# Kernel optimization log

Measured on AMD Instinct MI355X. Metric: run time of the kernel, lower is better.

The kernel has to match this reference:

```python
import jax, jax.numpy as jnp
import numpy as np

VOCAB, D, H, HK, DH, M, DFF, NCLS = 32000, 512, 8, 2, 64, 64, 2048, 2
G = H // HK  # GQA group size = 4
EPS = 1e-6


def rmsnorm(x, g):
    return x * jax.lax.rsqrt(jnp.mean(x * x, axis=-1, keepdims=True) + EPS) * g


def setup_inputs() -> dict:
    key = jax.random.key(0)
    ks = jax.random.split(key, 14)
    s = 0.02
    return {
        "input_ids": jax.random.randint(ks[0], (8, 8192), 0, VOCAB),
        "emb": jax.random.normal(ks[1], (VOCAB, D), jnp.float32) * s,
        "Wq": jax.random.normal(ks[2], (D, H * DH), jnp.float32) * s,
        "Wk": jax.random.normal(ks[3], (D, HK * DH), jnp.float32) * s,
        "Wv": jax.random.normal(ks[4], (D, HK * DH), jnp.float32) * s,
        "Wphi": jax.random.normal(ks[5], (DH, M), jnp.float32),  # Laplacian kernel feature projection
        "Wo": jax.random.normal(ks[6], (H * DH, D), jnp.float32) * s,
        "g1": jnp.ones((D,), jnp.float32),
        "g2": jnp.ones((D,), jnp.float32),
        "Wg": jax.random.normal(ks[7], (D, DFF), jnp.float32) * s,
        "Wu": jax.random.normal(ks[8], (D, DFF), jnp.float32) * s,  # frozen up_proj (freeze only affects training, not math)
        "Wd": jax.random.normal(ks[9], (DFF, D), jnp.float32) * s,
        "Wc": jax.random.normal(ks[10], (D, NCLS), jnp.float32) * s,
        "bc": jnp.zeros((NCLS,), jnp.float32),
    }


def reference(input_ids, emb, Wq, Wk, Wv, Wphi, Wo, g1, g2, Wg, Wu, Wd, Wc, bc):
    B, S = input_ids.shape
    x = emb[input_ids]  # [B,S,D] embedding gather
    # --- kernelized (Laplacian) bidirectional GQA linear attention, pre-norm ---
    h = rmsnorm(x, g1)
    q = (h @ Wq).reshape(B, S, H, DH)
    k = (h @ Wk).reshape(B, S, HK, DH)
    v = (h @ Wv).reshape(B, S, HK, DH)
    # Laplacian positive feature map: phi(u) = exp(-|u @ Wphi|)  -> [.., M]
    pq = jnp.exp(-jnp.abs(jnp.einsum("bshd,dm->bshm", q, Wphi)))
    pk = jnp.exp(-jnp.abs(jnp.einsum("bskd,dm->bskm", k, Wphi)))
    # global (bidirectional) state per kv head: [B,HK,M,DH] and normalizer [B,HK,M]
    kv = jnp.einsum("bskm,bskd->bkmd", pk, v)
    z = pk.sum(axis=1)
    pqg = pq.reshape(B, S, HK, G, M)  # group query heads onto kv heads
    num = jnp.einsum("bskgm,bkmd->bskgd", pqg, kv)
    den = jnp.einsum("bskgm,bkm->bskg", pqg, z)
    attn = (num / (den[..., None] + EPS)).reshape(B, S, H * DH)
    x = x + attn @ Wo
    # --- SwiGLU FFN, pre-norm ---
    h2 = rmsnorm(x, g2)
    x = x + (jax.nn.silu(h2 @ Wg) * (h2 @ Wu)) @ Wd
    # --- mean pool + linear head ---
    logits = x.mean(axis=1) @ Wc + bc  # [B, NCLS]
    return logits
```

## Files before the change

### kernel.cpp

```cpp
#include <hip/hip_runtime.h>
#include <hip/hip_bf16.h>
#include <math.h>

typedef __attribute__((ext_vector_type(8))) short bf16x8;
typedef __attribute__((ext_vector_type(4))) float f32x4;

#define DEV static __device__ __forceinline__
#define AS1 __attribute__((address_space(1)))
#define AS3 __attribute__((address_space(3)))

DEV float bf2f(__hip_bfloat16 v) { return __bfloat162float(v); }
DEV __hip_bfloat16 f2bf(float f) { return __float2bfloat16(f); }
DEV float us2f(unsigned short u) { return __uint_as_float(((unsigned int)u) << 16); }
DEV unsigned short f2us(float f) {
    __hip_bfloat16 b = __float2bfloat16(f);
    return *(unsigned short*)&b;
}

DEV void gload_lds16(const void* g, void* l) {
    __builtin_amdgcn_global_load_lds((const AS1 unsigned int*)g,
                                     (AS3 unsigned int*)l, 16, 0, 0);
}

DEV void load8(const void* p, size_t off, int f32m, float* o) {
    if (f32m) {
        const float4* r = (const float4*)((const float*)p + off);
        float4 A = r[0], B = r[1];
        o[0] = A.x; o[1] = A.y; o[2] = A.z; o[3] = A.w;
        o[4] = B.x; o[5] = B.y; o[6] = B.z; o[7] = B.w;
    } else {
        const ushort4* r = (const ushort4*)((const __hip_bfloat16*)p + off);
        ushort4 A = r[0], B = r[1];
        o[0] = us2f(A.x); o[1] = us2f(A.y); o[2] = us2f(A.z); o[3] = us2f(A.w);
        o[4] = us2f(B.x); o[5] = us2f(B.y); o[6] = us2f(B.z); o[7] = us2f(B.w);
    }
}

DEV float loadElem(const void* p, size_t idx, int f32m) {
    return f32m ? ((const float*)p)[idx] : bf2f(((const __hip_bfloat16*)p)[idx]);
}

constexpr int NTOK = 65536;

constexpr size_t OFF_WQPT = 0;
constexpr size_t OFF_WKPT = OFF_WQPT + 524288ull;
constexpr size_t OFF_WVT  = OFF_WKPT + 131072ull;
constexpr size_t OFF_WOT  = OFF_WVT  + 131072ull;
constexpr size_t OFF_WGT  = OFF_WOT  + 524288ull;
constexpr size_t OFF_WUT  = OFF_WGT  + 2097152ull;
constexpr size_t OFF_KV   = OFF_WUT  + 2097152ull;
constexpr size_t OFF_Z    = OFF_KV   + 262144ull;
constexpr size_t OFF_POOL = OFF_Z    + 4096ull;
constexpr size_t OFF_TSUM = OFF_POOL + 16384ull;
constexpr size_t OFF_FLAG = OFF_TSUM + 65536ull;
constexpr size_t PERSIST  = OFF_FLAG + 256ull;
constexpr size_t CHUNKBASE = PERSIST;
constexpr int    ZERO_FLOATS = (262144 + 4096 + 16384 + 65536) / 4;
constexpr size_t PERTOK = 4608ull;

__global__ __launch_bounds__(128) void detect_kernel(
    const unsigned int* __restrict__ w, int* __restrict__ flag)
{
    __shared__ int cnt;
    if (threadIdx.x == 0) cnt = 0;
    __syncthreads();
    unsigned int v = w[threadIdx.x];
    float a = fabsf(us2f((unsigned short)(v & 0xFFFFu)));
    if (a >= 0.0625f && a <= 8.0f) atomicAdd(&cnt, 1);
    __syncthreads();
    if (threadIdx.x == 0) *flag = (cnt < 64) ? 1 : 0;
}

__global__ __launch_bounds__(256) void zero_kernel(float* __restrict__ p, int n)
{
    int i = blockIdx.x * 256 + threadIdx.x;
    if (i < n) p[i] = 0.0f;
}

__global__ __launch_bounds__(256) void fuse_phi_kernel(
    const void* __restrict__ W, const void* __restrict__ Wphi,
    __hip_bfloat16* __restrict__ outT, int wld, const int* __restrict__ flag)
{
    const int f = *flag;
    int o = blockIdx.x * 256 + threadIdx.x;
    int hm = o >> 9, d = o & 511;
    int h = hm >> 6, m = hm & 63;
    float acc = 0.f;
    if (f) {
        const float* Wf = (const float*)W;
        const float* Pf = (const float*)Wphi;
        #pragma unroll 8
        for (int dh = 0; dh < 64; ++dh)
            acc += Wf[(size_t)d * wld + h * 64 + dh] * Pf[dh * 64 + m];
    } else {
        const __hip_bfloat16* Wb = (const __hip_bfloat16*)W;
        const __hip_bfloat16* Pb = (const __hip_bfloat16*)Wphi;
        #pragma unroll 8
        for (int dh = 0; dh < 64; ++dh)
            acc += bf2f(Wb[(size_t)d * wld + h * 64 + dh]) * bf2f(Pb[dh * 64 + m]);
    }
    outT[o] = f2bf(acc);
}

__global__ __launch_bounds__(256) void transpose_kernel(
    const void* __restrict__ src, __hip_bfloat16* __restrict__ dst, int R, int Ccols,
    const int* __restrict__ flag)
{
    __shared__ float tile[32][33];
    const int f = *flag;
    const int tx = threadIdx.x & 31, ty = threadIdx.x >> 5;
    const int c0 = blockIdx.x * 32, r0 = blockIdx.y * 32;
    #pragma unroll
    for (int k = 0; k < 4; ++k) {
        const int rl = ty + k * 8;
        tile[rl][tx] = loadElem(src, (size_t)(r0 + rl) * Ccols + c0 + tx, f);
    }
    __syncthreads();
    #pragma unroll
    for (int k = 0; k < 4; ++k) {
        const int cl = ty + k * 8;
        dst[(size_t)(c0 + cl) * R + r0 + tx] = f2bf(tile[tx][cl]);
    }
}

__global__ __launch_bounds__(256) void embed_rms_kernel(
    const int* __restrict__ ids, const void* __restrict__ emb,
    const void* __restrict__ g1, __hip_bfloat16* __restrict__ h,
    const int* __restrict__ flag)
{
    const int f = *flag;
    const int n = blockIdx.x * 4 + (threadIdx.x >> 6);
    const int lane = threadIdx.x & 63;
    const int id = ids[n];
    float x[8];
    load8(emb, (size_t)id * 512 + lane * 8, f, x);
    float ss = 0.f;
    #pragma unroll
    for (int i = 0; i < 8; ++i) ss += x[i] * x[i];
    #pragma unroll
    for (int off = 32; off; off >>= 1) ss += __shfl_xor(ss, off, 64);
    const float scale = rsqrtf(ss * (1.0f / 512.0f) + 1e-6f);
    float gv[8];
    load8(g1, (size_t)lane * 8, f, gv);
    ushort4 h0, h1;
    h0.x = f2us(x[0] * scale * gv[0]); h0.y = f2us(x[1] * scale * gv[1]);
    h0.z = f2us(x[2] * scale * gv[2]); h0.w = f2us(x[3] * scale * gv[3]);
    h1.x = f2us(x[4] * scale * gv[4]); h1.y = f2us(x[5] * scale * gv[5]);
    h1.z = f2us(x[6] * scale * gv[6]); h1.w = f2us(x[7] * scale * gv[7]);
    ushort4* ho = (ushort4*)(h + (size_t)n * 512 + lane * 8);
    ho[0] = h0; ho[1] = h1;
}

__global__ __launch_bounds__(256) void rms2_kernel(
    const float* __restrict__ xf, const void* __restrict__ g2,
    __hip_bfloat16* __restrict__ h, const int* __restrict__ flag)
{
    const int f = *flag;
    const int n = blockIdx.x * 4 + (threadIdx.x >> 6);
    const int lane = threadIdx.x & 63;
    const float4* xr = (const float4*)(xf + (size_t)n * 512);
    float4 a = xr[lane * 2], b = xr[lane * 2 + 1];
    float x[8] = { a.x, a.y, a.z, a.w, b.x, b.y, b.z, b.w };
    float ss = 0.f;
    #pragma unroll
    for (int i = 0; i < 8; ++i) ss += x[i] * x[i];
    #pragma unroll
    for (int off = 32; off; off >>= 1) ss += __shfl_xor(ss, off, 64);
    const float scale = rsqrtf(ss * (1.0f / 512.0f) + 1e-6f);
    float gv[8];
    load8(g2, (size_t)lane * 8, f, gv);
    ushort4 h0, h1;
    h0.x = f2us(x[0] * scale * gv[0]); h0.y = f2us(x[1] * scale * gv[1]);
    h0.z = f2us(x[2] * scale * gv[2]); h0.w = f2us(x[3] * scale * gv[3]);
    h1.x = f2us(x[4] * scale * gv[4]); h1.y = f2us(x[5] * scale * gv[5]);
    h1.z = f2us(x[6] * scale * gv[6]); h1.w = f2us(x[7] * scale * gv[7]);
    ushort4* ho = (ushort4*)(h + (size_t)n * 512 + lane * 8);
    ho[0] = h0; ho[1] = h1;
}

template<int MODE>
__global__ __launch_bounds__(256) void gemm128_kernel(
    const __hip_bfloat16* __restrict__ A, const __hip_bfloat16* __restrict__ Bt,
    float* __restrict__ xf, __hip_bfloat16* __restrict__ Cout2,
    float* __restrict__ pooled, const int* __restrict__ ids,
    const void* __restrict__ emb, const int* __restrict__ flag, int gbase, int K)
{
    __shared__ __align__(16) char As[8192];
    __shared__ __align__(16) char Bs[8192];
    __shared__ int idsL[128];

    const int tid = threadIdx.x;
    const int bm = blockIdx.x, bn = blockIdx.y;
    const int wave = tid >> 6, lane = tid & 63;
    const int quad = lane >> 4, lr = lane & 15;
    const int wm = (wave >> 1) << 6, wn = (wave & 1) << 6;

    if (MODE == 7 && tid < 128) idsL[tid] = ids[bm * 128 + tid];

    const int srow = (wave << 5) + (lane >> 2);
    const int scol = lane & 3;
    const int sfr  = (srow + (srow >> 2)) & 3;
    const int sofs = ((scol ^ sfr) << 3);

    const __hip_bfloat16* ga0 = A  + (size_t)(bm * 128 + srow) * K + sofs;
    const __hip_bfloat16* gb0 = Bt + (size_t)(bn * 128 + srow) * K + sofs;
    const __hip_bfloat16* ga1 = ga0 + (size_t)16 * K;
    const __hip_bfloat16* gb1 = gb0 + (size_t)16 * K;
    char* lA0 = As + (wave << 11);
    char* lA1 = lA0 + 1024;
    char* lB0 = Bs + (wave << 11);
    char* lB1 = lB0 + 1024;

    const int fl  = (lr + (lr >> 2)) & 3;
    const int ac  = (quad ^ fl) << 4;
    const char* arp = As + ((wm + lr) << 6) + ac;
    const char* brp = Bs + ((wn + lr) << 6) + ac;

    f32x4 acc[4][4];
    #pragma unroll
    for (int i = 0; i < 4; ++i)
        #pragma unroll
        for (int j = 0; j < 4; ++j)
            #pragma unroll
            for (int r = 0; r < 4; ++r) acc[i][j][r] = 0.0f;

    for (int k0 = 0; k0 < K; k0 += 32) {
        __syncthreads();
        gload_lds16(ga0 + k0, lA0);
        gload_lds16(ga1 + k0, lA1);
        gload_lds16(gb0 + k0, lB0);
        gload_lds16(gb1 + k0, lB1);
        __syncthreads();

        bf16x8 af[4], bfr[4];
        #pragma unroll
        for (int i = 0; i < 4; ++i)
            af[i] = *(const bf16x8*)(arp + i * 1024);
        #pragma unroll
        for (int j = 0; j < 4; ++j)
            bfr[j] = *(const bf16x8*)(brp + j * 1024);
        #pragma unroll
        for (int i = 0; i < 4; ++i)
            #pragma unroll
            for (int j = 0; j < 4; ++j)
                acc[i][j] = __builtin_amdgcn_mfma_f32_16x16x32_bf16(af[i], bfr[j], acc[i][j], 0, 0, 0);
    }

    const int col0 = bn * 128 + wn + lr;

    if (MODE == 7) {
        const int f = *flag;
        const int b = (gbase + bm * 128) >> 13;
        #pragma unroll
        for (int j = 0; j < 4; ++j) {
            const int col = col0 + j * 16;
            float s = 0.f;
            #pragma unroll
            for (int i = 0; i < 4; ++i)
                #pragma unroll
                for (int r = 0; r < 4; ++r) {
                    const int rl = wm + i * 16 + quad * 4 + r;
                    const float e = loadElem(emb, (size_t)idsL[rl] * 512 + col, f);
                    const float w = e + acc[i][j][r];
                    xf[(size_t)(bm * 128 + rl) * 512 + col] = w;
                    s += w;
                }
            s += __shfl_xor(s, 16, 64);
            s += __shfl_xor(s, 32, 64);
            if (quad == 0) atomicAdd(&pooled[b * 512 + col], s);
        }
        return;
    }

    const int row0 = bm * 128 + wm + quad * 4;
    #pragma unroll
    for (int i = 0; i < 4; ++i)
        #pragma unroll
        for (int j = 0; j < 4; ++j) {
            const int col = col0 + j * 16;
            #pragma unroll
            for (int r = 0; r < 4; ++r) {
                const int row = row0 + i * 16 + r;
                const float v = acc[i][j][r];
                Cout2[(size_t)row * 256 + col] = f2bf(bn == 0 ? expf(-fabsf(v)) : v);
            }
        }
}

__global__ __launch_bounds__(256, 2) void pq_mix_kernel(
    const __hip_bfloat16* __restrict__ h, const __hip_bfloat16* __restrict__ WQPt,
    const float* __restrict__ kvf, const float* __restrict__ zf,
    __hip_bfloat16* __restrict__ attn, int gbase, int K)
{
    __shared__ __align__(16) char As[8192];
    __shared__ __align__(16) char Bs[8192];
    __shared__ __align__(16) char Pl[128 * 272];
    __shared__ __align__(16) __hip_bfloat16 kvT[80][72];

    const int tid = threadIdx.x;
    const int bm = blockIdx.x, bn = blockIdx.y;
    const int kh = bn >> 1;
    const int wave = tid >> 6, lane = tid & 63;
    const int quad = lane >> 4, lr = lane & 15;
    const int wm = (wave >> 1) << 6, wn = (wave & 1) << 6;
    const int b = (gbase + bm * 128) >> 13;

    {
        const float* kvsrc = kvf + ((size_t)b * 2 + kh) * 4096;
        for (int i = tid; i < 4096; i += 256) {
            const int m = i >> 6, dh = i & 63;
            kvT[dh][m] = f2bf(kvsrc[i]);
        }
        if (tid < 64) kvT[64][tid] = f2bf(zf[((size_t)b * 2 + kh) * 64 + tid]);
        for (int i = tid; i < 15 * 64; i += 256)
            kvT[65 + (i >> 6)][i & 63] = f2bf(0.0f);
    }

    const int srow = (wave << 5) + (lane >> 2);
    const int scol = lane & 3;
    const int sfr  = (srow + (srow >> 2)) & 3;
    const int sofs = ((scol ^ sfr) << 3);

    const __hip_bfloat16* ga0 = h    + (size_t)(bm * 128 + srow) * K + sofs;
    const __hip_bfloat16* gb0 = WQPt + (size_t)(bn * 128 + srow) * K + sofs;
    const __hip_bfloat16* ga1 = ga0 + (size_t)16 * K;
    const __hip_bfloat16* gb1 = gb0 + (size_t)16 * K;
    char* lA0 = As + (wave << 11);
    char* lA1 = lA0 + 1024;
    char* lB0 = Bs + (wave << 11);
    char* lB1 = lB0 + 1024;

    const int fl  = (lr + (lr >> 2)) & 3;
    const int ac  = (quad ^ fl) << 4;
    const char* arp = As + ((wm + lr) << 6) + ac;
    const char* brp = Bs + ((wn + lr) << 6) + ac;

    f32x4 acc[4][4];
    #pragma unroll
    for (int i = 0; i < 4; ++i)
        #pragma unroll
        for (int j = 0; j < 4; ++j)
            #pragma unroll
            for (int r = 0; r < 4; ++r) acc[i][j][r] = 0.0f;

    for (int k0 = 0; k0 < K; k0 += 32) {
        __syncthreads();
        gload_lds16(ga0 + k0, lA0);
        gload_lds16(ga1 + k0, lA1);
        gload_lds16(gb0 + k0, lB0);
        gload_lds16(gb1 + k0, lB1);
        __syncthreads();

        bf16x8 af[4], bfr[4];
        #pragma unroll
        for (int i = 0; i < 4; ++i)
            af[i] = *(const bf16x8*)(arp + i * 1024);
        #pragma unroll
        for (int j = 0; j < 4; ++j)
            bfr[j] = *(const bf16x8*)(brp + j * 1024);
        #pragma unroll
        for (int i = 0; i < 4; ++i)
            #pragma unroll
            for (int j = 0; j < 4; ++j)
                acc[i][j] = __builtin_amdgcn_mfma_f32_16x16x32_bf16(af[i], bfr[j], acc[i][j], 0, 0, 0);
    }

    #pragma unroll
    for (int i = 0; i < 4; ++i)
        #pragma unroll
        for (int j = 0; j < 4; ++j)
            #pragma unroll
            for (int r = 0; r < 4; ++r) {
                const int rl = wm + i * 16 + quad * 4 + r;
                const int cl = wn + j * 16 + lr;
                *(__hip_bfloat16*)(Pl + rl * 272 + cl * 2) = f2bf(expf(-fabsf(acc[i][j][r])));
            }
    __syncthreads();

    const int hl = wave & 1;
    f32x4 acc2[4][5];
    #pragma unroll
    for (int i = 0; i < 4; ++i)
        #pragma unroll
        for (int j = 0; j < 5; ++j)
            #pragma unroll
            for (int r = 0; r < 4; ++r) acc2[i][j][r] = 0.0f;

    #pragma unroll
    for (int kk = 0; kk < 2; ++kk) {
        const int kofs = kk * 32 + quad * 8;
        bf16x8 af[4], bfr[5];
        #pragma unroll
        for (int i = 0; i < 4; ++i)
            af[i] = *(const bf16x8*)(Pl + (wm + i * 16 + lr) * 272 + (wn + kofs) * 2);
        #pragma unroll
        for (int j = 0; j < 5; ++j)
            bfr[j] = *(const bf16x8*)&kvT[j * 16 + lr][kofs];
        #pragma unroll
        for (int i = 0; i < 4; ++i)
            #pragma unroll
            for (int j = 0; j < 5; ++j)
                acc2[i][j] = __builtin_amdgcn_mfma_f32_16x16x32_bf16(af[i], bfr[j], acc2[i][j], 0, 0, 0);
    }

    const int colb = (bn * 2 + hl) * 64;
    #pragma unroll
    for (int i = 0; i < 4; ++i) {
        const int rowb = bm * 128 + wm + i * 16 + quad * 4;
        #pragma unroll
        for (int r = 0; r < 4; ++r) {
            const float den = __shfl(acc2[i][4][r], lane & 48, 64);
            const float inv = 1.0f / (den + 1e-6f);
            const size_t base = (size_t)(rowb + r) * 512 + colb;
            #pragma unroll
            for (int j = 0; j < 4; ++j)
                attn[base + j * 16 + lr] = f2bf(acc2[i][j][r] * inv);
        }
    }
}

__global__ __launch_bounds__(256, 2) void gemm_ffn_kernel(
    const __hip_bfloat16* __restrict__ A, const __hip_bfloat16* __restrict__ Bg,
    const __hip_bfloat16* __restrict__ Bu, float* __restrict__ tsum,
    int gbase, int K)
{
    __shared__ __align__(16) char As[16384];
    __shared__ __align__(16) char Gs[16384];
    __shared__ __align__(16) char Us[16384];

    const int tid = threadIdx.x;
    const int bm = blockIdx.x, bn = blockIdx.y;
    const int wave = tid >> 6, lane = tid & 63;
    const int quad = lane >> 4, lr = lane & 15;
    const int wm = (wave >> 1) << 6, wn = (wave & 1) << 6;

    const int srow = (wave << 5) + (lane >> 2);
    const int scol = lane & 3;
    const int sfr  = (srow + (srow >> 2)) & 3;
    const int sofs = ((scol ^ sfr) << 3);

    const __hip_bfloat16* ga0 = A  + (size_t)(bm * 128 + srow) * K + sofs;
    const __hip_bfloat16* gg0 = Bg + (size_t)(bn * 128 + srow) * K + sofs;
    const __hip_bfloat16* gu0 = Bu + (size_t)(bn * 128 + srow) * K + sofs;
    const __hip_bfloat16* ga1 = ga0 + (size_t)16 * K;
    const __hip_bfloat16* gg1 = gg0 + (size_t)16 * K;
    const __hip_bfloat16* gu1 = gu0 + (size_t)16 * K;
    char* lA0 = As + (wave << 11);
    char* lG0 = Gs + (wave << 11);
    char* lU0 = Us + (wave << 11);

    const int fl  = (lr + (lr >> 2)) & 3;
    const int ac  = (quad ^ fl) << 4;
    const char* arp = As + ((wm + lr) << 6) + ac;
    const char* grp = Gs + ((wn + lr) << 6) + ac;
    const char* urp = Us + ((wn + lr) << 6) + ac;

    f32x4 accG[4][4], accU[4][4];
    #pragma unroll
    for (int i = 0; i < 4; ++i)
        #pragma unroll
        for (int j = 0; j < 4; ++j)
            #pragma unroll
            for (int r = 0; r < 4; ++r) { accG[i][j][r] = 0.0f; accU[i][j][r] = 0.0f; }

    for (int k0 = 0; k0 < K; k0 += 64) {
        __syncthreads();
        gload_lds16(ga0 + k0,      lA0);
        gload_lds16(ga1 + k0,      lA0 + 1024);
        gload_lds16(ga0 + k0 + 32, lA0 + 8192);
        gload_lds16(ga1 + k0 + 32, lA0 + 8192 + 1024);
        gload_lds16(gg0 + k0,      lG0);
        gload_lds16(gg1 + k0,      lG0 + 1024);
        gload_lds16(gg0 + k0 + 32, lG0 + 8192);
        gload_lds16(gg1 + k0 + 32, lG0 + 8192 + 1024);
        gload_lds16(gu0 + k0,      lU0);
        gload_lds16(gu1 + k0,      lU0 + 1024);
        gload_lds16(gu0 + k0 + 32, lU0 + 8192);
        gload_lds16(gu1 + k0 + 32, lU0 + 8192 + 1024);
        __syncthreads();

        #pragma unroll
        for (int kk = 0; kk < 2; ++kk) {
            const int so = kk * 8192;
            bf16x8 af[4], bgf[4], buf_[4];
            #pragma unroll
            for (int i = 0; i < 4; ++i)
                af[i] = *(const bf16x8*)(arp + so + i * 1024);
            #pragma unroll
            for (int j = 0; j < 4; ++j) {
                bgf[j]  = *(const bf16x8*)(grp + so + j * 1024);
                buf_[j] = *(const bf16x8*)(urp + so + j * 1024);
            }
            #pragma unroll
            for (int i = 0; i < 4; ++i)
                #pragma unroll
                for (int j = 0; j < 4; ++j) {
                    accG[i][j] = __builtin_amdgcn_mfma_f32_16x16x32_bf16(af[i], bgf[j],  accG[i][j], 0, 0, 0);
                    accU[i][j] = __builtin_amdgcn_mfma_f32_16x16x32_bf16(af[i], buf_[j], accU[i][j], 0, 0, 0);
                }
        }
    }

    const int b = (gbase + bm * 128) >> 13;
    #pragma unroll
    for (int j = 0; j < 4; ++j) {
        float s = 0.f;
        #pragma unroll
        for (int i = 0; i < 4; ++i)
            #pragma unroll
            for (int r = 0; r < 4; ++r) {
                const float g = accG[i][j][r];
                s += (g / (1.0f + expf(-g))) * accU[i][j][r];
            }
        s += __shfl_xor(s, 16, 64);
        s += __shfl_xor(s, 32, 64);
        if (quad == 0)
            atomicAdd(&tsum[b * 2048 + bn * 128 + wn + lr + j * 16], s);
    }
}

__global__ __launch_bounds__(256) void ffn_pool_kernel(
    const float* __restrict__ tsum, const void* __restrict__ Wd,
    float* __restrict__ pooled, const int* __restrict__ flag)
{
    __shared__ float ts[8][64];
    const int f = *flag;
    const int k0 = blockIdx.x * 64;
    const int t = threadIdx.x;
    for (int i = t; i < 512; i += 256)
        ts[i >> 6][i & 63] = tsum[(i >> 6) * 2048 + k0 + (i & 63)];
    __syncthreads();

    float acc0[8] = {}, acc1[8] = {};
    for (int kk = 0; kk < 64; ++kk) {
        const size_t krow = (size_t)(k0 + kk) * 512;
        const float w0 = loadElem(Wd, krow + t, f);
        const float w1 = loadElem(Wd, krow + t + 256, f);
        #pragma unroll
        for (int b = 0; b < 8; ++b) {
            acc0[b] += ts[b][kk] * w0;
            acc1[b] += ts[b][kk] * w1;
        }
    }
    #pragma unroll
    for (int b = 0; b < 8; ++b) {
        atomicAdd(&pooled[b * 512 + t], acc0[b]);
        atomicAdd(&pooled[b * 512 + t + 256], acc1[b]);
    }
}

__global__ __launch_bounds__(256) void kv_z_kernel(
    const __hip_bfloat16* __restrict__ pkv,
    float* __restrict__ kv, float* __restrict__ z, int gbase, int nrows)
{
    __shared__ float pks[8][64], vs[8][64];
    const int slab = blockIdx.x, kh = blockIdx.y;
    const int b = (gbase + slab * nrows) >> 13;
    const int tid = threadIdx.x;
    const int tm = (tid & 15) << 2, tdh = (tid >> 4) << 2;
    const int lss = tid >> 5, lmm = (tid & 31) << 1;

    float acc[4][4] = {};
    float zacc[4] = {};
    for (int sb = 0; sb < nrows; sb += 8) {
        __syncthreads();
        {
            const size_t n = (size_t)slab * nrows + sb + lss;
            const __hip_bfloat16* pr = pkv + n * 256 + kh * 64 + lmm;
            const __hip_bfloat16* vr = pkv + n * 256 + 128 + kh * 64 + lmm;
            pks[lss][lmm]     = bf2f(pr[0]);
            pks[lss][lmm + 1] = bf2f(pr[1]);
            vs[lss][lmm]      = bf2f(vr[0]);
            vs[lss][lmm + 1]  = bf2f(vr[1]);
        }
        __syncthreads();
        #pragma unroll
        for (int ss = 0; ss < 8; ++ss) {
            f32x4 p = *(const f32x4*)&pks[ss][tm];
            f32x4 w = *(const f32x4*)&vs[ss][tdh];
            #pragma unroll
            for (int i = 0; i < 4; ++i)
                #pragma unroll
                for (int j = 0; j < 4; ++j)
                    acc[i][j] += p[i] * w[j];
            if ((tid >> 4) == 0) {
                #pragma unroll
                for (int i = 0; i < 4; ++i) zacc[i] += p[i];
            }
        }
    }
    #pragma unroll
    for (int i = 0; i < 4; ++i)
        #pragma unroll
        for (int j = 0; j < 4; ++j)
            atomicAdd(&kv[(((size_t)b * 2 + kh) * 64 + tm + i) * 64 + tdh + j], acc[i][j]);
    if ((tid >> 4) == 0) {
        #pragma unroll
        for (int i = 0; i < 4; ++i)
            atomicAdd(&z[((size_t)b * 2 + kh) * 64 + tm + i], zacc[i]);
    }
}

__global__ __launch_bounds__(256) void head_kernel(
    const float* __restrict__ pooled, const void* __restrict__ Wc,
    const void* __restrict__ bc, void* __restrict__ out, const int* __restrict__ flag)
{
    const int f = *flag;
    const int t = threadIdx.x;
    const int grp = t >> 4, ln = t & 15;
    const int b = grp >> 1, c = grp & 1;
    float p = 0.f;
    for (int d = ln; d < 512; d += 16)
        p += pooled[b * 512 + d] * loadElem(Wc, (size_t)d * 2 + c, f);
    #pragma unroll
    for (int off = 8; off; off >>= 1) p += __shfl_xor(p, off, 64);
    if (ln == 0) {
        const float val = p * (1.0f / 8192.0f) + loadElem(bc, c, f);
        if (f) ((float*)out)[b * 2 + c] = val;
        else   ((__hip_bfloat16*)out)[b * 2 + c] = f2bf(val);
    }
}

extern "C" void kernel_launch(void* const* d_in, const int* in_sizes, int n_in,
                              void* d_out, int out_size, void* d_ws, size_t ws_size,
                              hipStream_t stream)
{
    const int* ids   = (const int*)d_in[0];
    const void* emb  = d_in[1];
    const void* Wq   = d_in[2];
    const void* Wk   = d_in[3];
    const void* Wv   = d_in[4];
    const void* Wph  = d_in[5];
    const void* Wo   = d_in[6];
    const void* g1   = d_in[7];
    const void* g2   = d_in[8];
    const void* Wg   = d_in[9];
    const void* Wu   = d_in[10];
    const void* Wd   = d_in[11];
    const void* Wc   = d_in[12];
    const void* bc   = d_in[13];

    char* ws = (char*)d_ws;
    __hip_bfloat16* WQPt  = (__hip_bfloat16*)(ws + OFF_WQPT);
    __hip_bfloat16* WKPt  = (__hip_bfloat16*)(ws + OFF_WKPT);
    __hip_bfloat16* WvT   = (__hip_bfloat16*)(ws + OFF_WVT);
    __hip_bfloat16* WoT   = (__hip_bfloat16*)(ws + OFF_WOT);
    __hip_bfloat16* WgT   = (__hip_bfloat16*)(ws + OFF_WGT);
    __hip_bfloat16* WuT   = (__hip_bfloat16*)(ws + OFF_WUT);
    float*          kv    = (float*)(ws + OFF_KV);
    float*          z     = (float*)(ws + OFF_Z);
    float*          pooled= (float*)(ws + OFF_POOL);
    float*          tsum  = (float*)(ws + OFF_TSUM);
    int*            flag  = (int*)(ws + OFF_FLAG);

    int C = 32768;
    while (C > 256 && CHUNKBASE + PERTOK * (size_t)C > ws_size) C >>= 1;
    const int NC = NTOK / C;

    char* cb = ws + CHUNKBASE;
    float*          xf   = (float*)cb;
    __hip_bfloat16* h    = (__hip_bfloat16*)(cb + (size_t)C * 2048);
    __hip_bfloat16* attn = (__hip_bfloat16*)(cb + (size_t)C * 3072);
    __hip_bfloat16* pkv  = (__hip_bfloat16*)(cb + (size_t)C * 4096);

    detect_kernel<<<1, 128, 0, stream>>>((const unsigned int*)Wph, flag);
    zero_kernel<<<(ZERO_FLOATS + 255) / 256, 256, 0, stream>>>(kv, ZERO_FLOATS);

    fuse_phi_kernel<<<1024, 256, 0, stream>>>(Wq, Wph, WQPt, 512, flag);
    fuse_phi_kernel<<<256, 256, 0, stream>>>(Wk, Wph, WKPt, 128, flag);
    transpose_kernel<<<dim3(128 / 32, 512 / 32), 256, 0, stream>>>(Wv, WvT, 512, 128, flag);
    transpose_kernel<<<dim3(512 / 32, 512 / 32), 256, 0, stream>>>(Wo, WoT, 512, 512, flag);
    transpose_kernel<<<dim3(2048 / 32, 512 / 32), 256, 0, stream>>>(Wg, WgT, 512, 2048, flag);
    transpose_kernel<<<dim3(2048 / 32, 512 / 32), 256, 0, stream>>>(Wu, WuT, 512, 2048, flag);

    for (int c = 0; c < NC; ++c) {
        const int g0 = c * C;
        embed_rms_kernel<<<C / 4, 256, 0, stream>>>(ids + g0, emb, g1, h, flag);
        gemm128_kernel<8><<<dim3(C / 128, 2), 256, 0, stream>>>(
            h, WKPt, nullptr, pkv, nullptr, nullptr, nullptr, flag, g0, 512);
        kv_z_kernel<<<dim3(C / 128, 2), 256, 0, stream>>>(pkv, kv, z, g0, 128);
    }

    for (int c = 0; c < NC; ++c) {
        const int g0 = c * C;
        embed_rms_kernel<<<C / 4, 256, 0, stream>>>(ids + g0, emb, g1, h, flag);
        pq_mix_kernel<<<dim3(C / 128, 4), 256, 0, stream>>>(
            h, WQPt, kv, z, attn, g0, 512);
        gemm128_kernel<7><<<dim3(C / 128, 4), 256, 0, stream>>>(
            attn, WoT, xf, nullptr, pooled, ids + g0, emb, flag, g0, 512);
        rms2_kernel<<<C / 4, 256, 0, stream>>>(xf, g2, h, flag);
        dim3 gg(C / 128, 16);
        gemm_ffn_kernel<<<gg, 256, 0, stream>>>(h, WgT, WuT, tsum, g0, 512);
    }

    ffn_pool_kernel<<<32, 256, 0, stream>>>(tsum, Wd, pooled, flag);

    head_kernel<<<1, 256, 0, stream>>>(pooled, Wc, bc, d_out, flag);
}
```

Measured before the change: 968.6 us.

## Rewrite FFN GEMM as 8-wave double-buffered kernel and cache normalized activations

Replaces the 256-thread gate/up FFN GEMM with a 512-thread, 256x128 tile kernel. It double-buffers LDS across K steps, staggers global-to-LDS loads between phases, and raises MFMA priority with s_setprio. Each wave computes both gate and up columns in one accumulator array. It also stores the first-pass RMS-normalized activations for the full token range in a persistent buffer, so the second pass no longer re-runs embed_rms. The cost is 64 MB more workspace, which may shrink the chunk size, and 128 KB of LDS per block, which limits occupancy.

```diff
diff --git a/kernel.cpp b/kernel.cpp
--- a/kernel.cpp
+++ b/kernel.cpp
@@ -54,9 +54,10 @@
 constexpr size_t OFF_TSUM = OFF_POOL + 16384ull;
 constexpr size_t OFF_FLAG = OFF_TSUM + 65536ull;
 constexpr size_t PERSIST  = OFF_FLAG + 256ull;
-constexpr size_t CHUNKBASE = PERSIST;
+constexpr size_t OFF_H    = PERSIST;
+constexpr size_t CHUNKBASE = OFF_H + 67108864ull;
 constexpr int    ZERO_FLOATS = (262144 + 4096 + 16384 + 65536) / 4;
-constexpr size_t PERTOK = 4608ull;
+constexpr size_t PERTOK = 3584ull;
 
 __global__ __launch_bounds__(128) void detect_kernel(
     const unsigned int* __restrict__ w, int* __restrict__ flag)
@@ -419,103 +420,151 @@
     }
 }
 
-__global__ __launch_bounds__(256, 2) void gemm_ffn_kernel(
+__global__ __launch_bounds__(512, 2) void ffn8_kernel(
     const __hip_bfloat16* __restrict__ A, const __hip_bfloat16* __restrict__ Bg,
-    const __hip_bfloat16* __restrict__ Bu, float* __restrict__ tsum,
-    int gbase, int K)
-{
-    __shared__ __align__(16) char As[16384];
-    __shared__ __align__(16) char Gs[16384];
-    __shared__ __align__(16) char Us[16384];
+    const __hip_bfloat16* __restrict__ Bu, float* __restrict__ tsum, int gbase)
+{
+    __shared__ __align__(16) char L[131072];
 
     const int tid = threadIdx.x;
     const int bm = blockIdx.x, bn = blockIdx.y;
     const int wave = tid >> 6, lane = tid & 63;
     const int quad = lane >> 4, lr = lane & 15;
-    const int wm = (wave >> 1) << 6, wn = (wave & 1) << 6;
-
-    const int srow = (wave << 5) + (lane >> 2);
-    const int scol = lane & 3;
-    const int sfr  = (srow + (srow >> 2)) & 3;
-    const int sofs = ((scol ^ sfr) << 3);
-
-    const __hip_bfloat16* ga0 = A  + (size_t)(bm * 128 + srow) * K + sofs;
-    const __hip_bfloat16* gg0 = Bg + (size_t)(bn * 128 + srow) * K + sofs;
-    const __hip_bfloat16* gu0 = Bu + (size_t)(bn * 128 + srow) * K + sofs;
-    const __hip_bfloat16* ga1 = ga0 + (size_t)16 * K;
-    const __hip_bfloat16* gg1 = gg0 + (size_t)16 * K;
-    const __hip_bfloat16* gu1 = gu0 + (size_t)16 * K;
-    char* lA0 = As + (wave << 11);
-    char* lG0 = Gs + (wave << 11);
-    char* lU0 = Us + (wave << 11);
-
-    const int fl  = (lr + (lr >> 2)) & 3;
-    const int ac  = (quad ^ fl) << 4;
-    const char* arp = As + ((wm + lr) << 6) + ac;
-    const char* grp = Gs + ((wn + lr) << 6) + ac;
-    const char* urp = Us + ((wn + lr) << 6) + ac;
-
-    f32x4 accG[4][4], accU[4][4];
-    #pragma unroll
-    for (int i = 0; i < 4; ++i)
+    const int wm = (wave >> 2) << 7;
+    const int wn = (wave & 3) << 5;
+
+    const int trow = tid >> 3;
+    const int cswz = (((tid & 7) ^ (trow & 7)) << 3);
+    const __hip_bfloat16* gA0 = A  + (size_t)(bm * 256 + trow) * 512 + cswz;
+    const __hip_bfloat16* gG0 = Bg + (size_t)(bn * 128 + trow) * 512 + cswz;
+    const __hip_bfloat16* gU0 = Bu + (size_t)(bn * 128 + trow) * 512 + cswz;
+    const int ldsb = wave << 10;
+
+    const int sx = lr & 7;
+    const int s0 = (quad ^ sx) << 4;
+    const int s1 = ((quad + 4) ^ sx) << 4;
+    const int aro = (wm + lr) << 7;
+    const int bgo = 32768 + ((wn + lr) << 7);
+    const int buo = bgo + 16384;
+
+    f32x4 acc[8][4];
+    #pragma unroll
+    for (int m = 0; m < 8; ++m)
         #pragma unroll
         for (int j = 0; j < 4; ++j)
             #pragma unroll
-            for (int r = 0; r < 4; ++r) { accG[i][j][r] = 0.0f; accU[i][j][r] = 0.0f; }
-
-    for (int k0 = 0; k0 < K; k0 += 64) {
-        __syncthreads();
-        gload_lds16(ga0 + k0,      lA0);
-        gload_lds16(ga1 + k0,      lA0 + 1024);
-        gload_lds16(ga0 + k0 + 32, lA0 + 8192);
-        gload_lds16(ga1 + k0 + 32, lA0 + 8192 + 1024);
-        gload_lds16(gg0 + k0,      lG0);
-        gload_lds16(gg1 + k0,      lG0 + 1024);
-        gload_lds16(gg0 + k0 + 32, lG0 + 8192);
-        gload_lds16(gg1 + k0 + 32, lG0 + 8192 + 1024);
-        gload_lds16(gu0 + k0,      lU0);
-        gload_lds16(gu1 + k0,      lU0 + 1024);
-        gload_lds16(gu0 + k0 + 32, lU0 + 8192);
-        gload_lds16(gu1 + k0 + 32, lU0 + 8192 + 1024);
-        __syncthreads();
-
-        #pragma unroll
-        for (int kk = 0; kk < 2; ++kk) {
-            const int so = kk * 8192;
-            bf16x8 af[4], bgf[4], buf_[4];
-            #pragma unroll
-            for (int i = 0; i < 4; ++i)
-                af[i] = *(const bf16x8*)(arp + so + i * 1024);
-            #pragma unroll
-            for (int j = 0; j < 4; ++j) {
-                bgf[j]  = *(const bf16x8*)(grp + so + j * 1024);
-                buf_[j] = *(const bf16x8*)(urp + so + j * 1024);
-            }
-            #pragma unroll
-            for (int i = 0; i < 4; ++i)
-                #pragma unroll
-                for (int j = 0; j < 4; ++j) {
-                    accG[i][j] = __builtin_amdgcn_mfma_f32_16x16x32_bf16(af[i], bgf[j],  accG[i][j], 0, 0, 0);
-                    accU[i][j] = __builtin_amdgcn_mfma_f32_16x16x32_bf16(af[i], buf_[j], accU[i][j], 0, 0, 0);
-                }
-        }
-    }
-
-    const int b = (gbase + bm * 128) >> 13;
-    #pragma unroll
-    for (int j = 0; j < 4; ++j) {
+            for (int r = 0; r < 4; ++r) acc[m][j][r] = 0.0f;
+
+    #pragma unroll
+    for (int l = 0; l < 4; ++l)
+        gload_lds16(gA0 + (size_t)l * 32768, L + l * 8192 + ldsb);
+    gload_lds16(gG0,         L + 32768 + ldsb);
+    gload_lds16(gG0 + 32768, L + 40960 + ldsb);
+    gload_lds16(gU0,         L + 49152 + ldsb);
+    gload_lds16(gU0 + 32768, L + 57344 + ldsb);
+
+    for (int t = 0; t < 8; ++t) {
+        const char* cbuf = L + ((t & 1) << 16);
+        char* nbuf = (char*)L + (((t + 1) & 1) << 16);
+        const int kn = (t + 1) << 6;
+        bf16x8 af[4], bfv[4];
+
+        if (t < 7) {
+            #pragma unroll
+            for (int l = 0; l < 4; ++l)
+                gload_lds16(gA0 + (size_t)l * 32768 + kn, nbuf + l * 8192 + ldsb);
+            asm volatile("s_waitcnt vmcnt(4)" ::: "memory");
+        } else {
+            asm volatile("s_waitcnt vmcnt(0)" ::: "memory");
+        }
+        __builtin_amdgcn_s_barrier();
+        asm volatile("" ::: "memory");
+        #pragma unroll
+        for (int m = 0; m < 4; ++m) af[m] = *(const bf16x8*)(cbuf + aro + m * 2048 + s0);
+        bfv[0] = *(const bf16x8*)(cbuf + bgo + s0);
+        bfv[1] = *(const bf16x8*)(cbuf + bgo + 2048 + s0);
+        bfv[2] = *(const bf16x8*)(cbuf + buo + s0);
+        bfv[3] = *(const bf16x8*)(cbuf + buo + 2048 + s0);
+        asm volatile("s_waitcnt lgkmcnt(0)" ::: "memory");
+        __builtin_amdgcn_s_setprio(1);
+        #pragma unroll
+        for (int m = 0; m < 4; ++m)
+            #pragma unroll
+            for (int j = 0; j < 4; ++j)
+                acc[m][j] = __builtin_amdgcn_mfma_f32_16x16x32_bf16(af[m], bfv[j], acc[m][j], 0, 0, 0);
+        __builtin_amdgcn_s_setprio(0);
+        asm volatile("" ::: "memory");
+        __builtin_amdgcn_s_barrier();
+        asm volatile("" ::: "memory");
+
+        if (t < 7) {
+            gload_lds16(gG0 + kn,         nbuf + 32768 + ldsb);
+            gload_lds16(gG0 + 32768 + kn, nbuf + 40960 + ldsb);
+            gload_lds16(gU0 + kn,         nbuf + 49152 + ldsb);
+            gload_lds16(gU0 + 32768 + kn, nbuf + 57344 + ldsb);
+        }
+        #pragma unroll
+        for (int m = 0; m < 4; ++m) af[m] = *(const bf16x8*)(cbuf + aro + (m + 4) * 2048 + s0);
+        asm volatile("s_waitcnt lgkmcnt(0)" ::: "memory");
+        __builtin_amdgcn_s_setprio(1);
+        #pragma unroll
+        for (int m = 0; m < 4; ++m)
+            #pragma unroll
+            for (int j = 0; j < 4; ++j)
+                acc[m + 4][j] = __builtin_amdgcn_mfma_f32_16x16x32_bf16(af[m], bfv[j], acc[m + 4][j], 0, 0, 0);
+        __builtin_amdgcn_s_setprio(0);
+        asm volatile("" ::: "memory");
+        __builtin_amdgcn_s_barrier();
+        asm volatile("" ::: "memory");
+
+        #pragma unroll
+        for (int m = 0; m < 4; ++m) af[m] = *(const bf16x8*)(cbuf + aro + m * 2048 + s1);
+        bfv[0] = *(const bf16x8*)(cbuf + bgo + s1);
+        bfv[1] = *(const bf16x8*)(cbuf + bgo + 2048 + s1);
+        bfv[2] = *(const bf16x8*)(cbuf + buo + s1);
+        bfv[3] = *(const bf16x8*)(cbuf + buo + 2048 + s1);
+        asm volatile("s_waitcnt lgkmcnt(0)" ::: "memory");
+        __builtin_amdgcn_s_setprio(1);
+        #pragma unroll
+        for (int m = 0; m < 4; ++m)
+            #pragma unroll
+            for (int j = 0; j < 4; ++j)
+                acc[m][j] = __builtin_amdgcn_mfma_f32_16x16x32_bf16(af[m], bfv[j], acc[m][j], 0, 0, 0);
+        __builtin_amdgcn_s_setprio(0);
+        asm volatile("" ::: "memory");
+        __builtin_amdgcn_s_barrier();
+        asm volatile("" ::: "memory");
+
+        #pragma unroll
+        for (int m = 0; m < 4; ++m) af[m] = *(const bf16x8*)(cbuf + aro + (m + 4) * 2048 + s1);
+        asm volatile("s_waitcnt lgkmcnt(0)" ::: "memory");
+        __builtin_amdgcn_s_setprio(1);
+        #pragma unroll
+        for (int m = 0; m < 4; ++m)
+            #pragma unroll
+            for (int j = 0; j < 4; ++j)
+                acc[m + 4][j] = __builtin_amdgcn_mfma_f32_16x16x32_bf16(af[m], bfv[j], acc[m + 4][j], 0, 0, 0);
+        __builtin_amdgcn_s_setprio(0);
+        asm volatile("" ::: "memory");
+        __builtin_amdgcn_s_barrier();
+        asm volatile("" ::: "memory");
+    }
+
+    const int b = (gbase + bm * 256) >> 13;
+    #pragma unroll
+    for (int j = 0; j < 2; ++j) {
         float s = 0.f;
         #pragma unroll
-        for (int i = 0; i < 4; ++i)
+        for (int m = 0; m < 8; ++m)
             #pragma unroll
             for (int r = 0; r < 4; ++r) {
-                const float g = accG[i][j][r];
-                s += (g / (1.0f + expf(-g))) * accU[i][j][r];
+                const float g = acc[m][j][r];
+                s += (g / (1.0f + expf(-g))) * acc[m][j + 2][r];
             }
         s += __shfl_xor(s, 16, 64);
         s += __shfl_xor(s, 32, 64);
         if (quad == 0)
-            atomicAdd(&tsum[b * 2048 + bn * 128 + wn + lr + j * 16], s);
+            atomicAdd(&tsum[b * 2048 + bn * 128 + wn + j * 16 + lr], s);
     }
 }
 
@@ -652,6 +701,7 @@
     float*          pooled= (float*)(ws + OFF_POOL);
     float*          tsum  = (float*)(ws + OFF_TSUM);
     int*            flag  = (int*)(ws + OFF_FLAG);
+    __hip_bfloat16* hall  = (__hip_bfloat16*)(ws + OFF_H);
 
     int C = 32768;
     while (C > 256 && CHUNKBASE + PERTOK * (size_t)C > ws_size) C >>= 1;
@@ -659,9 +709,8 @@
 
     char* cb = ws + CHUNKBASE;
     float*          xf   = (float*)cb;
-    __hip_bfloat16* h    = (__hip_bfloat16*)(cb + (size_t)C * 2048);
-    __hip_bfloat16* attn = (__hip_bfloat16*)(cb + (size_t)C * 3072);
-    __hip_bfloat16* pkv  = (__hip_bfloat16*)(cb + (size_t)C * 4096);
+    __hip_bfloat16* attn = (__hip_bfloat16*)(cb + (size_t)C * 2048);
+    __hip_bfloat16* pkv  = (__hip_bfloat16*)(cb + (size_t)C * 3072);
 
     detect_kernel<<<1, 128, 0, stream>>>((const unsigned int*)Wph, flag);
     zero_kernel<<<(ZERO_FLOATS + 255) / 256, 256, 0, stream>>>(kv, ZERO_FLOATS);
@@ -675,22 +724,22 @@
 
     for (int c = 0; c < NC; ++c) {
         const int g0 = c * C;
-        embed_rms_kernel<<<C / 4, 256, 0, stream>>>(ids + g0, emb, g1, h, flag);
+        __hip_bfloat16* hc = hall + (size_t)g0 * 512;
+        embed_rms_kernel<<<C / 4, 256, 0, stream>>>(ids + g0, emb, g1, hc, flag);
         gemm128_kernel<8><<<dim3(C / 128, 2), 256, 0, stream>>>(
-            h, WKPt, nullptr, pkv, nullptr, nullptr, nullptr, flag, g0, 512);
+            hc, WKPt, nullptr, pkv, nullptr, nullptr, nullptr, flag, g0, 512);
         kv_z_kernel<<<dim3(C / 128, 2), 256, 0, stream>>>(pkv, kv, z, g0, 128);
     }
 
     for (int c = 0; c < NC; ++c) {
         const int g0 = c * C;
-        embed_rms_kernel<<<C / 4, 256, 0, stream>>>(ids + g0, emb, g1, h, flag);
+        __hip_bfloat16* hc = hall + (size_t)g0 * 512;
         pq_mix_kernel<<<dim3(C / 128, 4), 256, 0, stream>>>(
-            h, WQPt, kv, z, attn, g0, 512);
+            hc, WQPt, kv, z, attn, g0, 512);
         gemm128_kernel<7><<<dim3(C / 128, 4), 256, 0, stream>>>(
             attn, WoT, xf, nullptr, pooled, ids + g0, emb, flag, g0, 512);
-        rms2_kernel<<<C / 4, 256, 0, stream>>>(xf, g2, h, flag);
-        dim3 gg(C / 128, 16);
-        gemm_ffn_kernel<<<gg, 256, 0, stream>>>(h, WgT, WuT, tsum, g0, 512);
+        rms2_kernel<<<C / 4, 256, 0, stream>>>(xf, g2, hc, flag);
+        ffn8_kernel<<<dim3(C / 256, 16), 512, 0, stream>>>(hc, WgT, WuT, tsum, g0);
     }
 
     ffn_pool_kernel<<<32, 256, 0, stream>>>(tsum, Wd, pooled, flag);
```

After: 963.2 us. About the same (-0.6%).

## Keep normed activations across passes and restructure FFN GEMM with full-K A tile in LDS

Applied to the files above, without the earlier changes.

The normed hidden states from the first pass are now stored in a persistent 64MB buffer, so the second pass no longer recomputes the embedding gather and RMSNorm. The FFN gate/up GEMM is rewritten so that each 512-thread block loads its full 128x512 A tile into 128KB of LDS once. Each of its 8 waves then streams Wg/Wu columns directly from global memory and covers the whole 2048-wide FFN width, which removes re-reading A from global memory for each of 16 N-tiles. The costs are much higher LDS use (one block per CU), B operands read from global without LDS staging, a larger workspace requirement that may force smaller chunks, and fewer blocks in the grid.

```diff
diff --git a/kernel.cpp b/kernel.cpp
--- a/kernel.cpp
+++ b/kernel.cpp
@@ -54,9 +54,10 @@
 constexpr size_t OFF_TSUM = OFF_POOL + 16384ull;
 constexpr size_t OFF_FLAG = OFF_TSUM + 65536ull;
 constexpr size_t PERSIST  = OFF_FLAG + 256ull;
-constexpr size_t CHUNKBASE = PERSIST;
+constexpr size_t OFF_H    = PERSIST;
+constexpr size_t CHUNKBASE = OFF_H + 67108864ull;
 constexpr int    ZERO_FLOATS = (262144 + 4096 + 16384 + 65536) / 4;
-constexpr size_t PERTOK = 4608ull;
+constexpr size_t PERTOK = 3584ull;
 
 __global__ __launch_bounds__(128) void detect_kernel(
     const unsigned int* __restrict__ w, int* __restrict__ flag)
@@ -419,103 +420,85 @@
     }
 }
 
-__global__ __launch_bounds__(256, 2) void gemm_ffn_kernel(
+__global__ __launch_bounds__(512, 2) void ffn8_kernel(
     const __hip_bfloat16* __restrict__ A, const __hip_bfloat16* __restrict__ Bg,
-    const __hip_bfloat16* __restrict__ Bu, float* __restrict__ tsum,
-    int gbase, int K)
-{
-    __shared__ __align__(16) char As[16384];
-    __shared__ __align__(16) char Gs[16384];
-    __shared__ __align__(16) char Us[16384];
+    const __hip_bfloat16* __restrict__ Bu, float* __restrict__ tsum, int gbase)
+{
+    __shared__ __align__(16) char L[131072];
 
     const int tid = threadIdx.x;
-    const int bm = blockIdx.x, bn = blockIdx.y;
+    const int bm = blockIdx.x;
     const int wave = tid >> 6, lane = tid & 63;
     const int quad = lane >> 4, lr = lane & 15;
-    const int wm = (wave >> 1) << 6, wn = (wave & 1) << 6;
-
-    const int srow = (wave << 5) + (lane >> 2);
-    const int scol = lane & 3;
-    const int sfr  = (srow + (srow >> 2)) & 3;
-    const int sofs = ((scol ^ sfr) << 3);
-
-    const __hip_bfloat16* ga0 = A  + (size_t)(bm * 128 + srow) * K + sofs;
-    const __hip_bfloat16* gg0 = Bg + (size_t)(bn * 128 + srow) * K + sofs;
-    const __hip_bfloat16* gu0 = Bu + (size_t)(bn * 128 + srow) * K + sofs;
-    const __hip_bfloat16* ga1 = ga0 + (size_t)16 * K;
-    const __hip_bfloat16* gg1 = gg0 + (size_t)16 * K;
-    const __hip_bfloat16* gu1 = gu0 + (size_t)16 * K;
-    char* lA0 = As + (wave << 11);
-    char* lG0 = Gs + (wave << 11);
-    char* lU0 = Us + (wave << 11);
-
-    const int fl  = (lr + (lr >> 2)) & 3;
-    const int ac  = (quad ^ fl) << 4;
-    const char* arp = As + ((wm + lr) << 6) + ac;
-    const char* grp = Gs + ((wn + lr) << 6) + ac;
-    const char* urp = Us + ((wn + lr) << 6) + ac;
-
-    f32x4 accG[4][4], accU[4][4];
-    #pragma unroll
-    for (int i = 0; i < 4; ++i)
-        #pragma unroll
-        for (int j = 0; j < 4; ++j)
-            #pragma unroll
-            for (int r = 0; r < 4; ++r) { accG[i][j][r] = 0.0f; accU[i][j][r] = 0.0f; }
-
-    for (int k0 = 0; k0 < K; k0 += 64) {
-        __syncthreads();
-        gload_lds16(ga0 + k0,      lA0);
-        gload_lds16(ga1 + k0,      lA0 + 1024);
-        gload_lds16(ga0 + k0 + 32, lA0 + 8192);
-        gload_lds16(ga1 + k0 + 32, lA0 + 8192 + 1024);
-        gload_lds16(gg0 + k0,      lG0);
-        gload_lds16(gg1 + k0,      lG0 + 1024);
-        gload_lds16(gg0 + k0 + 32, lG0 + 8192);
-        gload_lds16(gg1 + k0 + 32, lG0 + 8192 + 1024);
-        gload_lds16(gu0 + k0,      lU0);
-        gload_lds16(gu1 + k0,      lU0 + 1024);
-        gload_lds16(gu0 + k0 + 32, lU0 + 8192);
-        gload_lds16(gu1 + k0 + 32, lU0 + 8192 + 1024);
-        __syncthreads();
-
-        #pragma unroll
-        for (int kk = 0; kk < 2; ++kk) {
-            const int so = kk * 8192;
-            bf16x8 af[4], bgf[4], buf_[4];
-            #pragma unroll
-            for (int i = 0; i < 4; ++i)
-                af[i] = *(const bf16x8*)(arp + so + i * 1024);
-            #pragma unroll
-            for (int j = 0; j < 4; ++j) {
-                bgf[j]  = *(const bf16x8*)(grp + so + j * 1024);
-                buf_[j] = *(const bf16x8*)(urp + so + j * 1024);
+
+    {
+        const int ss = (lane & 56) | ((lane ^ wave) & 7);
+        const __hip_bfloat16* gsrc = A + (size_t)(bm * 128 + wave) * 512 + ss * 8;
+        char* ldst = L + wave * 1024;
+        #pragma unroll
+        for (int i = 0; i < 16; ++i)
+            gload_lds16(gsrc + (size_t)i * 8 * 512, ldst + i * 8192);
+    }
+    asm volatile("s_waitcnt vmcnt(0)" ::: "memory");
+    __syncthreads();
+
+    const int x7s = (lr & 7) << 4;
+    const char* ap = L + (lr << 10) + (((quad << 4) ^ x7s) & 0x70) + ((quad << 4) & ~0x70);
+    const char* apq = L + (lr << 10);
+
+    const __hip_bfloat16* pG = Bg + (size_t)(wave * 256 + lr) * 512 + quad * 8;
+    const __hip_bfloat16* pU = Bu + (size_t)(wave * 256 + lr) * 512 + quad * 8;
+
+    const int b = (gbase + bm * 128) >> 13;
+    (void)ap;
+
+    for (int ci = 0; ci < 8; ++ci) {
+        const __hip_bfloat16* pGc = pG + (size_t)ci * 32 * 512;
+        const __hip_bfloat16* pUc = pU + (size_t)ci * 32 * 512;
+
+        f32x4 aG[8][2], aU[8][2];
+        #pragma unroll
+        for (int m = 0; m < 8; ++m)
+            #pragma unroll
+            for (int c = 0; c < 2; ++c)
+                #pragma unroll
+                for (int r = 0; r < 4; ++r) { aG[m][c][r] = 0.0f; aU[m][c][r] = 0.0f; }
+
+        #pragma unroll 2
+        for (int ks = 0; ks < 16; ++ks) {
+            const int so = ((ks << 6) | (quad << 4)) ^ x7s;
+            bf16x8 af[8];
+            #pragma unroll
+            for (int m = 0; m < 8; ++m)
+                af[m] = *(const bf16x8*)(apq + m * 16384 + so);
+            bf16x8 bg0 = *(const bf16x8*)(pGc + ks * 32);
+            bf16x8 bg1 = *(const bf16x8*)(pGc + 16 * 512 + ks * 32);
+            bf16x8 bu0 = *(const bf16x8*)(pUc + ks * 32);
+            bf16x8 bu1 = *(const bf16x8*)(pUc + 16 * 512 + ks * 32);
+            #pragma unroll
+            for (int m = 0; m < 8; ++m) {
+                aG[m][0] = __builtin_amdgcn_mfma_f32_16x16x32_bf16(af[m], bg0, aG[m][0], 0, 0, 0);
+                aG[m][1] = __builtin_amdgcn_mfma_f32_16x16x32_bf16(af[m], bg1, aG[m][1], 0, 0, 0);
+                aU[m][0] = __builtin_amdgcn_mfma_f32_16x16x32_bf16(af[m], bu0, aU[m][0], 0, 0, 0);
+                aU[m][1] = __builtin_amdgcn_mfma_f32_16x16x32_bf16(af[m], bu1, aU[m][1], 0, 0, 0);
             }
-            #pragma unroll
-            for (int i = 0; i < 4; ++i)
+        }
+
+        #pragma unroll
+        for (int c = 0; c < 2; ++c) {
+            float s = 0.f;
+            #pragma unroll
+            for (int m = 0; m < 8; ++m)
                 #pragma unroll
-                for (int j = 0; j < 4; ++j) {
-                    accG[i][j] = __builtin_amdgcn_mfma_f32_16x16x32_bf16(af[i], bgf[j],  accG[i][j], 0, 0, 0);
-                    accU[i][j] = __builtin_amdgcn_mfma_f32_16x16x32_bf16(af[i], buf_[j], accU[i][j], 0, 0, 0);
+                for (int r = 0; r < 4; ++r) {
+                    const float g = aG[m][c][r];
+                    s += (g / (1.0f + expf(-g))) * aU[m][c][r];
                 }
-        }
-    }
-
-    const int b = (gbase + bm * 128) >> 13;
-    #pragma unroll
-    for (int j = 0; j < 4; ++j) {
-        float s = 0.f;
-        #pragma unroll
-        for (int i = 0; i < 4; ++i)
-            #pragma unroll
-            for (int r = 0; r < 4; ++r) {
-                const float g = accG[i][j][r];
-                s += (g / (1.0f + expf(-g))) * accU[i][j][r];
-            }
-        s += __shfl_xor(s, 16, 64);
-        s += __shfl_xor(s, 32, 64);
-        if (quad == 0)
-            atomicAdd(&tsum[b * 2048 + bn * 128 + wn + lr + j * 16], s);
+            s += __shfl_xor(s, 16, 64);
+            s += __shfl_xor(s, 32, 64);
+            if (quad == 0)
+                atomicAdd(&tsum[b * 2048 + wave * 256 + ci * 32 + c * 16 + lr], s);
+        }
     }
 }
 
@@ -652,6 +635,7 @@
     float*          pooled= (float*)(ws + OFF_POOL);
     float*          tsum  = (float*)(ws + OFF_TSUM);
     int*            flag  = (int*)(ws + OFF_FLAG);
+    __hip_bfloat16* hall  = (__hip_bfloat16*)(ws + OFF_H);
 
     int C = 32768;
     while (C > 256 && CHUNKBASE + PERTOK * (size_t)C > ws_size) C >>= 1;
@@ -659,9 +643,8 @@
 
     char* cb = ws + CHUNKBASE;
     float*          xf   = (float*)cb;
-    __hip_bfloat16* h    = (__hip_bfloat16*)(cb + (size_t)C * 2048);
-    __hip_bfloat16* attn = (__hip_bfloat16*)(cb + (size_t)C * 3072);
-    __hip_bfloat16* pkv  = (__hip_bfloat16*)(cb + (size_t)C * 4096);
+    __hip_bfloat16* attn = (__hip_bfloat16*)(cb + (size_t)C * 2048);
+    __hip_bfloat16* pkv  = (__hip_bfloat16*)(cb + (size_t)C * 3072);
 
     detect_kernel<<<1, 128, 0, stream>>>((const unsigned int*)Wph, flag);
     zero_kernel<<<(ZERO_FLOATS + 255) / 256, 256, 0, stream>>>(kv, ZERO_FLOATS);
@@ -675,22 +658,22 @@
 
     for (int c = 0; c < NC; ++c) {
         const int g0 = c * C;
-        embed_rms_kernel<<<C / 4, 256, 0, stream>>>(ids + g0, emb, g1, h, flag);
+        __hip_bfloat16* hc = hall + (size_t)g0 * 512;
+        embed_rms_kernel<<<C / 4, 256, 0, stream>>>(ids + g0, emb, g1, hc, flag);
         gemm128_kernel<8><<<dim3(C / 128, 2), 256, 0, stream>>>(
-            h, WKPt, nullptr, pkv, nullptr, nullptr, nullptr, flag, g0, 512);
+            hc, WKPt, nullptr, pkv, nullptr, nullptr, nullptr, flag, g0, 512);
         kv_z_kernel<<<dim3(C / 128, 2), 256, 0, stream>>>(pkv, kv, z, g0, 128);
     }
 
     for (int c = 0; c < NC; ++c) {
         const int g0 = c * C;
-        embed_rms_kernel<<<C / 4, 256, 0, stream>>>(ids + g0, emb, g1, h, flag);
+        __hip_bfloat16* hc = hall + (size_t)g0 * 512;
         pq_mix_kernel<<<dim3(C / 128, 4), 256, 0, stream>>>(
-            h, WQPt, kv, z, attn, g0, 512);
+            hc, WQPt, kv, z, attn, g0, 512);
         gemm128_kernel<7><<<dim3(C / 128, 4), 256, 0, stream>>>(
             attn, WoT, xf, nullptr, pooled, ids + g0, emb, flag, g0, 512);
-        rms2_kernel<<<C / 4, 256, 0, stream>>>(xf, g2, h, flag);
-        dim3 gg(C / 128, 16);
-        gemm_ffn_kernel<<<gg, 256, 0, stream>>>(h, WgT, WuT, tsum, g0, 512);
+        rms2_kernel<<<C / 4, 256, 0, stream>>>(xf, g2, hc, flag);
+        ffn8_kernel<<<C / 128, 512, 0, stream>>>(hc, WgT, WuT, tsum, g0);
     }
 
     ffn_pool_kernel<<<32, 256, 0, stream>>>(tsum, Wd, pooled, flag);
```

New measurement: 933.7 us. -3.6%, faster.
